# Kernel tuning notes

Measured on AMD Instinct MI355X. Metric: run time of the kernel, lower is better.

## Reference

```python
import jax, jax.numpy as jnp
import numpy as np

D, B, N, DIM, H, DH, MLP = 6, 4, 1024, 768, 12, 64, 3072
SCALE = DH ** -0.5
EPS = 1e-5


def setup_inputs() -> dict:
    key = jax.random.key(0)
    ks = jax.random.split(key, 5)
    s = 0.02
    return {
        "x": jax.random.normal(ks[0], (B, N, DIM), jnp.float32),
        "ln1_g": jnp.ones((D, DIM), jnp.float32),
        "ln1_b": jnp.zeros((D, DIM), jnp.float32),
        "wqkv": jax.random.normal(ks[1], (D, DIM, 3 * H * DH), jnp.float32) * s,
        "wo": jax.random.normal(ks[2], (D, H * DH, DIM), jnp.float32) * s,
        "bo": jnp.zeros((D, DIM), jnp.float32),
        "ln2_g": jnp.ones((D, DIM), jnp.float32),
        "ln2_b": jnp.zeros((D, DIM), jnp.float32),
        "w1": jax.random.normal(ks[3], (D, DIM, MLP), jnp.float32) * s,
        "b1": jnp.zeros((D, MLP), jnp.float32),
        "w2": jax.random.normal(ks[4], (D, MLP, DIM), jnp.float32) * s,
        "b2": jnp.zeros((D, DIM), jnp.float32),
    }


def _ln(h, g, b):
    m = h.mean(-1, keepdims=True)
    v = h.var(-1, keepdims=True)  # biased, matches torch LayerNorm
    return (h - m) / jnp.sqrt(v + EPS) * g + b


def _heads(t):
    # [b, n, h*d] -> [b, h, n, d]
    return t.reshape(B, N, H, DH).transpose(0, 2, 1, 3)


def reference(x, ln1_g, ln1_b, wqkv, wo, bo, ln2_g, ln2_b, w1, b1, w2, b2):
    def step(carry, p):
        xc, _, _ = carry
        g1, be1, Wqkv, Wo, Bo, g2, be2, W1, B1, W2, B2 = p
        h = _ln(xc, g1, be1)
        q, k, v = jnp.split(h @ Wqkv, 3, axis=-1)
        q, k, v = _heads(q), _heads(k), _heads(v)
        attn = jax.nn.softmax(jnp.einsum('bhid,bhjd->bhij', q, k) * SCALE, axis=-1)
        out = jnp.einsum('bhij,bhjd->bhid', attn, v)
        out = out.transpose(0, 2, 1, 3).reshape(B, N, H * DH)
        xc = xc + out @ Wo + Bo
        h2 = _ln(xc, g2, be2)
        xc = xc + jax.nn.gelu(h2 @ W1 + B1, approximate=False) @ W2 + B2
        return (xc, k, v), None

    kv0 = jnp.zeros((B, H, N, DH), x.dtype)
    (xf, k, v), _ = jax.lax.scan(
        step, (x, kv0, kv0),
        (ln1_g, ln1_b, wqkv, wo, bo, ln2_g, ln2_b, w1, b1, w2, b2))
    return xf, k, v
```

## Files before the change

kernel.cpp:

```cpp
#include <hip/hip_runtime.h>
#include <hip/hip_bf16.h>
#include <math.h>

typedef __bf16 bf16;
typedef __bf16 bf16x8 __attribute__((ext_vector_type(8)));
typedef float f32x4 __attribute__((ext_vector_type(4)));

enum { EPI_QKV = 0, EPI_GELU = 1 };

__device__ __forceinline__ void gload16(const void* g, void* s) {
  __builtin_amdgcn_global_load_lds((__attribute__((address_space(1))) void*)g,
                                   (__attribute__((address_space(3))) void*)s, 16, 0, 0);
}

#define MFMA16(a, b, c) __builtin_amdgcn_mfma_f32_16x16x32_bf16((a), (b), (c), 0, 0, 0)

__device__ __forceinline__ void xcd_swizzle(int& bx, int& by) {
  const int gx = gridDim.x, nwg = gx * gridDim.y;
  int bid = blockIdx.y * gx + blockIdx.x;
  if ((nwg & 7) == 0) bid = (bid & 7) * (nwg >> 3) + (bid >> 3);
  bx = bid % gx;
  by = bid / gx;
}

__global__ __launch_bounds__(256) void cast_x(const float* __restrict__ x,
                                              float* __restrict__ xq) {
  const int i = (blockIdx.x * 256 + threadIdx.x) * 4;
  float4 v = *(const float4*)(x + i);
  v.x = (float)(bf16)v.x; v.y = (float)(bf16)v.y;
  v.z = (float)(bf16)v.z; v.w = (float)(bf16)v.w;
  *(float4*)(xq + i) = v;
}

__global__ __launch_bounds__(256) void wconv_all(
    const float* __restrict__ wqkv, const float* __restrict__ wo,
    const float* __restrict__ w1, const float* __restrict__ w2,
    bf16* __restrict__ qkvT, bf16* __restrict__ woT,
    bf16* __restrict__ w1T, bf16* __restrict__ w2T, int lfix) {
  __shared__ float tile[64][65];
  const int bid = blockIdx.x, t = threadIdx.x;
  int l, r;
  if (lfix < 0) { l = bid / 1728; r = bid % 1728; } else { l = lfix; r = bid; }
  const int lo = (lfix < 0) ? l : 0;
  const float* W; bf16* Wt; int K, N, tt;
  if (r < 432)       { W = wqkv + (size_t)l * 768 * 2304; Wt = qkvT + (size_t)lo * 2304 * 768; K = 768;  N = 2304; tt = r; }
  else if (r < 576)  { W = wo   + (size_t)l * 768 * 768;  Wt = woT  + (size_t)lo * 768 * 768;  K = 768;  N = 768;  tt = r - 432; }
  else if (r < 1152) { W = w1   + (size_t)l * 768 * 3072; Wt = w1T  + (size_t)lo * 3072 * 768; K = 768;  N = 3072; tt = r - 576; }
  else               { W = w2   + (size_t)l * 3072 * 768; Wt = w2T  + (size_t)lo * 768 * 3072; K = 3072; N = 768;  tt = r - 1152; }
  const int ntx = N >> 6;
  const int n0 = (tt % ntx) * 64, k0 = (tt / ntx) * 64;
  const int cx = (t & 15) * 4, ry = t >> 4;
#pragma unroll
  for (int pp = 0; pp < 4; ++pp) {
    const int row = ry + pp * 16;
    const float4 v = *(const float4*)(W + (size_t)(k0 + row) * N + n0 + cx);
    tile[row][cx] = v.x; tile[row][cx + 1] = v.y;
    tile[row][cx + 2] = v.z; tile[row][cx + 3] = v.w;
  }
  __syncthreads();
#pragma unroll
  for (int it = 0; it < 2; ++it) {
    const int c = it * 256 + t;
    const int n = c >> 3, kc = (c & 7) * 8;
    bf16x8 v;
#pragma unroll
    for (int j = 0; j < 8; ++j) v[j] = (bf16)tile[kc + j][n];
    *(bf16x8*)(Wt + (size_t)(n0 + n) * K + k0 + kc) = v;
  }
}

__global__ __launch_bounds__(256) void ln_kernel(const float* __restrict__ x,
                                                 const float* __restrict__ g,
                                                 const float* __restrict__ b,
                                                 bf16* __restrict__ out) {
  const int row = blockIdx.x, t = threadIdx.x;
  const float* xr = x + (size_t)row * 768;
  float v0 = xr[t], v1 = xr[t + 256], v2 = xr[t + 512];
  float s = v0 + v1 + v2, sq = v0 * v0 + v1 * v1 + v2 * v2;
#pragma unroll
  for (int m = 32; m; m >>= 1) { s += __shfl_xor(s, m); sq += __shfl_xor(sq, m); }
  __shared__ float rs[4], rq[4];
  const int w = t >> 6;
  if ((t & 63) == 0) { rs[w] = s; rq[w] = sq; }
  __syncthreads();
  s = rs[0] + rs[1] + rs[2] + rs[3];
  sq = rq[0] + rq[1] + rq[2] + rq[3];
  const float mean = s * (1.f / 768.f);
  const float var = sq * (1.f / 768.f) - mean * mean;
  const float rstd = rsqrtf(var + 1e-5f);
  bf16* orow = out + (size_t)row * 768;
  orow[t]       = (bf16)((v0 - mean) * rstd * g[t]       + b[t]);
  orow[t + 256] = (bf16)((v1 - mean) * rstd * g[t + 256] + b[t + 256]);
  orow[t + 512] = (bf16)((v2 - mean) * rstd * g[t + 512] + b[t + 512]);
}

template <int EPI>
__global__ __launch_bounds__(256) void gemm_s(
    const bf16* __restrict__ A, const bf16* __restrict__ Bt,
    const float* __restrict__ bias, bf16* __restrict__ Cb,
    bf16* __restrict__ qo, bf16* __restrict__ ko_, bf16* __restrict__ vo,
    float* __restrict__ kf, float* __restrict__ vf, int wf,
    int M, int Nc, int K) {
  __shared__ __align__(16) char lds[2][2][8192];
  const int t = threadIdx.x, lane = t & 63, w = t >> 6;
  const int wr = w >> 1, wc = w & 1;
  int bx, by;
  xcd_swizzle(bx, by);
  const size_t m0 = (size_t)by * 128, n0 = (size_t)bx * 128;

  const char* ab[2]; const char* bb[2];
#pragma unroll
  for (int r = 0; r < 2; ++r) {
    int c = r * 256 + t;
    ab[r] = (const char*)(A + (m0 + (c >> 2)) * (size_t)K) + (c & 3) * 16;
    bb[r] = (const char*)(Bt + (n0 + (c >> 2)) * (size_t)K) + (c & 3) * 16;
  }

  f32x4 acc[4][4] = {};

  auto stage = [&](int buf, int tt) {
#pragma unroll
    for (int r = 0; r < 2; ++r) {
      gload16(ab[r] + (size_t)tt * 64, &lds[buf][0][r * 4096 + w * 1024]);
      gload16(bb[r] + (size_t)tt * 64, &lds[buf][1][r * 4096 + w * 1024]);
    }
  };
  auto compute = [&](int buf) {
    const char* As = lds[buf][0];
    const char* Bs = lds[buf][1];
    const int ko = (lane >> 4) * 16;
    bf16x8 af[4], fb[4];
#pragma unroll
    for (int i = 0; i < 4; ++i) {
      af[i] = *(const bf16x8*)(As + (wr * 64 + i * 16 + (lane & 15)) * 64 + ko);
      fb[i] = *(const bf16x8*)(Bs + (wc * 64 + i * 16 + (lane & 15)) * 64 + ko);
    }
#pragma unroll
    for (int mi = 0; mi < 4; ++mi)
#pragma unroll
      for (int ni = 0; ni < 4; ++ni)
        acc[mi][ni] = MFMA16(af[mi], fb[ni], acc[mi][ni]);
  };

  const int NT = K >> 5;
  stage(0, 0);
  __syncthreads();
  int cur = 0;
  for (int tt = 1; tt < NT; ++tt) {
    stage(cur ^ 1, tt);
    compute(cur);
    __syncthreads();
    cur ^= 1;
  }
  compute(cur);

#pragma unroll
  for (int mi = 0; mi < 4; ++mi) {
#pragma unroll
    for (int i = 0; i < 4; ++i) {
      size_t row = m0 + wr * 64 + mi * 16 + ((lane >> 4) << 2) + i;
#pragma unroll
      for (int ni = 0; ni < 4; ++ni) {
        size_t col = n0 + wc * 64 + ni * 16 + (lane & 15);
        float v = acc[mi][ni][i];
        if (EPI == EPI_GELU) {
          v += bias[col];
          v = 0.5f * v * (1.f + erff(v * 0.70710678118f));
          Cb[row * (size_t)Nc + col] = (bf16)v;
        } else {
          int b = (int)(row >> 10), n = (int)(row & 1023);
          int which = (int)col >= 1536 ? 2 : ((int)col >= 768 ? 1 : 0);
          int hd = (int)col - which * 768;
          int hh = hd >> 6, d = hd & 63;
          size_t dst = ((size_t)(b * 12 + hh) * 1024 + n) * 64 + d;
          if (which == 0) {
            qo[dst] = (bf16)(v * 0.125f);
          } else if (which == 1) {
            ko_[dst] = (bf16)v;
            if (wf) kf[dst] = v;
          } else {
            vo[dst] = (bf16)v;
            if (wf) vf[dst] = v;
          }
        }
      }
    }
  }
}

__global__ __launch_bounds__(256) void gemm64_s(
    const bf16* __restrict__ A, const bf16* __restrict__ Bt,
    const float* __restrict__ bias, const float* __restrict__ res,
    float* __restrict__ Cf, int M, int Nc, int K) {
  __shared__ __align__(16) char lds[2][12288];
  const int t = threadIdx.x, lane = t & 63, w = t >> 6;
  const int wr = w >> 1, wc = w & 1;
  const int l15 = lane & 15, l4 = lane >> 4;
  int bx, by;
  xcd_swizzle(bx, by);
  const size_t m0 = (size_t)by * 64, n0 = (size_t)bx * 128;

  const char* ab = (const char*)(A + (m0 + (t >> 2)) * (size_t)K) + (t & 3) * 16;
  const char* b0 = (const char*)(Bt + (n0 + (t >> 2)) * (size_t)K) + (t & 3) * 16;
  const char* b1 = (const char*)(Bt + (n0 + 64 + (t >> 2)) * (size_t)K) + (t & 3) * 16;

  f32x4 acc[2][4] = {};

  auto stage = [&](int buf, int tt) {
    gload16(ab + (size_t)tt * 64, &lds[buf][t * 16]);
    gload16(b0 + (size_t)tt * 64, &lds[buf][4096 + t * 16]);
    gload16(b1 + (size_t)tt * 64, &lds[buf][8192 + t * 16]);
  };
  auto compute = [&](int buf) {
    const char* L = lds[buf];
    const int ko = l4 * 16;
    bf16x8 fa[2], fb[4];
#pragma unroll
    for (int mi = 0; mi < 2; ++mi)
      fa[mi] = *(const bf16x8*)(L + (wr * 32 + mi * 16 + l15) * 64 + ko);
#pragma unroll
    for (int ni = 0; ni < 4; ++ni)
      fb[ni] = *(const bf16x8*)(L + 4096 + (wc * 64 + ni * 16 + l15) * 64 + ko);
#pragma unroll
    for (int mi = 0; mi < 2; ++mi)
#pragma unroll
      for (int ni = 0; ni < 4; ++ni)
        acc[mi][ni] = MFMA16(fa[mi], fb[ni], acc[mi][ni]);
  };

  const int NT = K >> 5;
  stage(0, 0);
  __syncthreads();
  int cur = 0;
  for (int tt = 1; tt < NT; ++tt) {
    stage(cur ^ 1, tt);
    compute(cur);
    __syncthreads();
    cur ^= 1;
  }
  compute(cur);

#pragma unroll
  for (int mi = 0; mi < 2; ++mi) {
#pragma unroll
    for (int i = 0; i < 4; ++i) {
      size_t row = m0 + wr * 32 + mi * 16 + l4 * 4 + i;
#pragma unroll
      for (int ni = 0; ni < 4; ++ni) {
        size_t col = n0 + wc * 64 + ni * 16 + l15;
        float v = acc[mi][ni][i] + bias[col] + res[row * (size_t)Nc + col];
        Cf[row * (size_t)Nc + col] = v;
      }
    }
  }
}

__global__ __launch_bounds__(256) void vtrans(const bf16* __restrict__ v,
                                              bf16* __restrict__ vT) {
  __shared__ bf16 tile[32][33];
  const int tx = threadIdx.x, ty = threadIdx.y;
  const int bh = blockIdx.x, n0 = blockIdx.y * 32, d0 = blockIdx.z * 32;
  const bf16* vb = v + (size_t)bh * 1024 * 64;
  bf16* vTb = vT + (size_t)bh * 64 * 1024;
#pragma unroll
  for (int r = 0; r < 4; ++r)
    tile[ty + r * 8][tx] = vb[(size_t)(n0 + ty + r * 8) * 64 + d0 + tx];
  __syncthreads();
#pragma unroll
  for (int r = 0; r < 4; ++r)
    vTb[(size_t)(d0 + ty + r * 8) * 1024 + n0 + tx] = tile[tx][ty + r * 8];
}

__global__ __launch_bounds__(64) void attn_kernel(const bf16* __restrict__ q,
                                                  const bf16* __restrict__ k,
                                                  const bf16* __restrict__ vT,
                                                  bf16* __restrict__ out) {
  __shared__ __align__(16) char Ks[16384];
  __shared__ __align__(16) char Vs[16384];
  char* Ps = Ks;
  const int bh = blockIdx.x, qb = blockIdx.y;
  const int lane = threadIdx.x & 63;
  const int l15 = lane & 15, l4 = lane >> 4;

  const char* kp = (const char*)(k + (size_t)bh * 1024 * 64);
  const char* vp = (const char*)(vT + (size_t)bh * 64 * 1024);

  const char* kb0 = kp + (lane >> 3) * 128 + (((lane & 7) ^ ((lane >> 3) & 7)) * 16);
  const int vr0 = lane >> 4;
  const char* vb0 = vp + (size_t)vr0 * 2048 + (((lane & 15) ^ vr0) * 16);
  const char* vb1 = vp + (size_t)(vr0 + 4) * 2048 + (((lane & 15) ^ (vr0 + 4)) * 16);

  bf16x8 aq[2][2];
  {
    const bf16* qbase = q + ((size_t)bh * 1024 + qb * 32) * 64;
#pragma unroll
    for (int mi = 0; mi < 2; ++mi)
#pragma unroll
      for (int ks = 0; ks < 2; ++ks)
        aq[mi][ks] = *(const bf16x8*)(qbase + (mi * 16 + l15) * 64 + ks * 32 + l4 * 8);
  }

  bf16x8 vones;
#pragma unroll
  for (int j = 0; j < 8; ++j) vones[j] = (bf16)1.0f;

  f32x4 oacc[2][4] = {};
  f32x4 lacc[2] = {};
  float mrun[2][4];
#pragma unroll
  for (int mi = 0; mi < 2; ++mi)
#pragma unroll
    for (int i = 0; i < 4; ++i) mrun[mi][i] = -1e30f;

  for (int kb = 0; kb < 8; ++kb) {
    const char* ksrc = kb0 + (size_t)kb * 16384;
#pragma unroll
    for (int r = 0; r < 16; ++r)
      gload16(ksrc + r * 1024, &Ks[r * 1024]);
    const char* vsrc0 = vb0 + kb * 256;
    const char* vsrc1 = vb1 + kb * 256;
#pragma unroll
    for (int r = 0; r < 8; ++r) {
      gload16(vsrc0 + (size_t)r * 16384, &Vs[r * 2048]);
      gload16(vsrc1 + (size_t)r * 16384, &Vs[r * 2048 + 1024]);
    }
    asm volatile("s_waitcnt vmcnt(16)" ::: "memory");
    __builtin_amdgcn_sched_barrier(0);

    f32x4 sacc[2][8] = {};
#pragma unroll
    for (int ks = 0; ks < 2; ++ks) {
#pragma unroll
      for (int ni = 0; ni < 8; ++ni) {
        const int rr = ni * 16 + l15;
        const bf16x8 bk = *(const bf16x8*)(Ks + rr * 128 + (((ks * 4 + l4) ^ (rr & 7)) * 16));
        sacc[0][ni] = MFMA16(aq[0][ks], bk, sacc[0][ni]);
        sacc[1][ni] = MFMA16(aq[1][ks], bk, sacc[1][ni]);
      }
    }

#pragma unroll
    for (int mi = 0; mi < 2; ++mi) {
#pragma unroll
      for (int i = 0; i < 4; ++i) {
        float mx = sacc[mi][0][i];
#pragma unroll
        for (int ni = 1; ni < 8; ++ni) mx = fmaxf(mx, sacc[mi][ni][i]);
#pragma unroll
        for (int sh = 8; sh; sh >>= 1) mx = fmaxf(mx, __shfl_xor(mx, sh));
        float mnew = fmaxf(mrun[mi][i], mx);
        float alpha = __expf(mrun[mi][i] - mnew);
        mrun[mi][i] = mnew;
#pragma unroll
        for (int ni = 0; ni < 8; ++ni)
          sacc[mi][ni][i] = __expf(sacc[mi][ni][i] - mnew);
#pragma unroll
        for (int ni = 0; ni < 4; ++ni) oacc[mi][ni][i] *= alpha;
        lacc[mi][i] *= alpha;
      }
    }

#pragma unroll
    for (int mi = 0; mi < 2; ++mi)
#pragma unroll
      for (int i = 0; i < 4; ++i) {
        int rowl = mi * 16 + l4 * 4 + i;
        char* prp = Ps + rowl * 256;
        int sw = rowl & 7;
#pragma unroll
        for (int ni = 0; ni < 8; ++ni) {
          int col = ni * 16 + l15;
          *(bf16*)(prp + (((col >> 3) ^ sw) * 16) + (col & 7) * 2) = (bf16)sacc[mi][ni][i];
        }
      }

    asm volatile("s_waitcnt vmcnt(0)" ::: "memory");
    __builtin_amdgcn_sched_barrier(0);

    const int prow0 = l15, prow1 = 16 + l15;
#pragma unroll
    for (int ks = 0; ks < 4; ++ks) {
      const bf16x8 ap0 = *(const bf16x8*)(Ps + prow0 * 256 + (((ks * 4 + l4) ^ (prow0 & 7)) * 16));
      const bf16x8 ap1 = *(const bf16x8*)(Ps + prow1 * 256 + (((ks * 4 + l4) ^ (prow1 & 7)) * 16));
#pragma unroll
      for (int ni = 0; ni < 4; ++ni) {
        const int vr = ni * 16 + l15;
        const bf16x8 bv = *(const bf16x8*)(Vs + vr * 256 + (((ks * 4 + l4) ^ (vr & 7)) * 16));
        oacc[0][ni] = MFMA16(ap0, bv, oacc[0][ni]);
        oacc[1][ni] = MFMA16(ap1, bv, oacc[1][ni]);
      }
      lacc[0] = MFMA16(ap0, vones, lacc[0]);
      lacc[1] = MFMA16(ap1, vones, lacc[1]);
    }
  }

  const int b = bh / 12, hh = bh % 12;
#pragma unroll
  for (int mi = 0; mi < 2; ++mi)
#pragma unroll
    for (int i = 0; i < 4; ++i) {
      int n = qb * 32 + mi * 16 + l4 * 4 + i;
      float inv = 1.f / lacc[mi][i];
      bf16* orow = out + ((size_t)b * 1024 + n) * 768 + hh * 64;
#pragma unroll
      for (int ni = 0; ni < 4; ++ni)
        orow[ni * 16 + l15] = (bf16)(oacc[mi][ni][i] * inv);
    }
}

extern "C" void kernel_launch(void* const* d_in, const int* in_sizes, int n_in,
                              void* d_out, int out_size, void* d_ws, size_t ws_size,
                              hipStream_t stream) {
  (void)in_sizes; (void)n_in; (void)out_size;
  const float* x_in = (const float*)d_in[0];
  const float* ln1g = (const float*)d_in[1];
  const float* ln1b = (const float*)d_in[2];
  const float* wqkv = (const float*)d_in[3];
  const float* wo   = (const float*)d_in[4];
  const float* bo   = (const float*)d_in[5];
  const float* ln2g = (const float*)d_in[6];
  const float* ln2b = (const float*)d_in[7];
  const float* w1   = (const float*)d_in[8];
  const float* b1   = (const float*)d_in[9];
  const float* w2   = (const float*)d_in[10];
  const float* b2   = (const float*)d_in[11];

  float* outx = (float*)d_out;
  float* outk = outx + (size_t)4096 * 768;
  float* outv = outk + (size_t)4096 * 768;

  char* p = (char*)d_ws;
  auto take = [&](size_t bytes) {
    char* r = p;
    p += (bytes + 255) & ~(size_t)255;
    return r;
  };
  float* xw   = (float*)take((size_t)4096 * 768 * 4);
  bf16*  h    = (bf16*)take((size_t)4096 * 768 * 2);
  bf16*  mbuf = (bf16*)take((size_t)4096 * 3072 * 2);
  bf16*  qbuf = (bf16*)take((size_t)4096 * 768 * 2);
  bf16*  kbuf = (bf16*)take((size_t)4096 * 768 * 2);
  bf16*  vbuf = (bf16*)take((size_t)4096 * 768 * 2);
  bf16*  vTb  = (bf16*)take((size_t)4096 * 768 * 2);
  bf16*  abuf = (bf16*)take((size_t)4096 * 768 * 2);

  const size_t wq1 = (size_t)2304 * 768, wo1 = (size_t)768 * 768,
               w11 = (size_t)3072 * 768, w21 = (size_t)768 * 3072;
  const size_t used = (size_t)(p - (char*)d_ws);
  const size_t wbytes = (wq1 + wo1 + w11 + w21) * 2;
  const bool hoist = ws_size >= used + 6 * wbytes + 8192;
  const int nl = hoist ? 6 : 1;
  bf16* qkvT = (bf16*)take(wq1 * 2 * nl);
  bf16* woT  = (bf16*)take(wo1 * 2 * nl);
  bf16* w1T  = (bf16*)take(w11 * 2 * nl);
  bf16* w2T  = (bf16*)take(w21 * 2 * nl);

  cast_x<<<3072, 256, 0, stream>>>(x_in, xw);
  if (hoist)
    wconv_all<<<10368, 256, 0, stream>>>(wqkv, wo, w1, w2, qkvT, woT, w1T, w2T, -1);

  for (int l = 0; l < 6; ++l) {
    if (!hoist)
      wconv_all<<<1728, 256, 0, stream>>>(wqkv, wo, w1, w2, qkvT, woT, w1T, w2T, l);
    bf16* qkL = qkvT + (hoist ? (size_t)l * wq1 : 0);
    bf16* woL = woT  + (hoist ? (size_t)l * wo1 : 0);
    bf16* w1L = w1T  + (hoist ? (size_t)l * w11 : 0);
    bf16* w2L = w2T  + (hoist ? (size_t)l * w21 : 0);

    ln_kernel<<<4096, 256, 0, stream>>>(xw, ln1g + l * 768, ln1b + l * 768, h);
    gemm_s<EPI_QKV><<<dim3(18, 32), 256, 0, stream>>>(
        h, qkL, nullptr, nullptr, qbuf, kbuf, vbuf, outk, outv, l == 5 ? 1 : 0,
        4096, 2304, 768);
    vtrans<<<dim3(48, 32, 2), dim3(32, 8), 0, stream>>>(vbuf, vTb);
    attn_kernel<<<dim3(48, 32), 64, 0, stream>>>(qbuf, kbuf, vTb, abuf);
    gemm64_s<<<dim3(6, 64), 256, 0, stream>>>(
        abuf, woL, bo + l * 768, xw, xw, 4096, 768, 768);
    ln_kernel<<<4096, 256, 0, stream>>>(xw, ln2g + l * 768, ln2b + l * 768, h);
    gemm_s<EPI_GELU><<<dim3(24, 32), 256, 0, stream>>>(
        h, w1L, b1 + l * 3072, mbuf, nullptr, nullptr, nullptr, nullptr, nullptr, 0,
        4096, 3072, 768);
    gemm64_s<<<dim3(6, 64), 256, 0, stream>>>(
        mbuf, w2L, b2 + l * 768, xw, (l == 5) ? outx : xw, 4096, 768, 3072);
  }
}
```

Measured before the change: 1.270 ms.

## Split attention over key halves with a separate log-sum-exp combine kernel

```diff
diff --git a/kernel.cpp b/kernel.cpp
--- a/kernel.cpp
+++ b/kernel.cpp
@@ -271,24 +271,28 @@
     vTb[(size_t)(d0 + ty + r * 8) * 1024 + n0 + tx] = tile[tx][ty + r * 8];
 }
 
-__global__ __launch_bounds__(64) void attn_kernel(const bf16* __restrict__ q,
-                                                  const bf16* __restrict__ k,
-                                                  const bf16* __restrict__ vT,
-                                                  bf16* __restrict__ out) {
+__global__ __launch_bounds__(64) void attn_main(const bf16* __restrict__ q,
+                                                const bf16* __restrict__ k,
+                                                const bf16* __restrict__ vT,
+                                                float* __restrict__ pO,
+                                                float* __restrict__ pM,
+                                                float* __restrict__ pL) {
   __shared__ __align__(16) char Ks[16384];
   __shared__ __align__(16) char Vs[16384];
   char* Ps = Ks;
-  const int bh = blockIdx.x, qb = blockIdx.y;
+  const int bh = blockIdx.x, qb = blockIdx.y, half = blockIdx.z;
   const int lane = threadIdx.x & 63;
   const int l15 = lane & 15, l4 = lane >> 4;
 
   const char* kp = (const char*)(k + (size_t)bh * 1024 * 64);
   const char* vp = (const char*)(vT + (size_t)bh * 64 * 1024);
 
-  const char* kb0 = kp + (lane >> 3) * 128 + (((lane & 7) ^ ((lane >> 3) & 7)) * 16);
+  const char* kb0 = kp + (lane >> 3) * 128 + (((lane & 7) ^ ((lane >> 3) & 7)) * 16)
+                  + (size_t)half * 4 * 16384;
   const int vr0 = lane >> 4;
-  const char* vb0 = vp + (size_t)vr0 * 2048 + (((lane & 15) ^ vr0) * 16);
-  const char* vb1 = vp + (size_t)(vr0 + 4) * 2048 + (((lane & 15) ^ (vr0 + 4)) * 16);
+  const char* vb0 = vp + (size_t)vr0 * 2048 + (((lane & 15) ^ vr0) * 16) + half * 4 * 256;
+  const char* vb1 = vp + (size_t)(vr0 + 4) * 2048 + (((lane & 15) ^ (vr0 + 4)) * 16)
+                  + half * 4 * 256;
 
   bf16x8 aq[2][2];
   {
@@ -312,13 +316,14 @@
 #pragma unroll
     for (int i = 0; i < 4; ++i) mrun[mi][i] = -1e30f;
 
-  for (int kb = 0; kb < 8; ++kb) {
-    const char* ksrc = kb0 + (size_t)kb * 16384;
+#pragma unroll
+  for (int jb = 0; jb < 4; ++jb) {
+    const char* ksrc = kb0 + (size_t)jb * 16384;
 #pragma unroll
     for (int r = 0; r < 16; ++r)
       gload16(ksrc + r * 1024, &Ks[r * 1024]);
-    const char* vsrc0 = vb0 + kb * 256;
-    const char* vsrc1 = vb1 + kb * 256;
+    const char* vsrc0 = vb0 + jb * 256;
+    const char* vsrc1 = vb1 + jb * 256;
 #pragma unroll
     for (int r = 0; r < 8; ++r) {
       gload16(vsrc0 + (size_t)r * 16384, &Vs[r * 2048]);
@@ -394,18 +399,47 @@
     }
   }
 
+  const size_t pb = ((size_t)half * 1536 + bh * 32 + qb) * 32;
+#pragma unroll
+  for (int mi = 0; mi < 2; ++mi)
+#pragma unroll
+    for (int i = 0; i < 4; ++i) {
+      const int row = mi * 16 + l4 * 4 + i;
+      float* po = pO + (pb + row) * 64;
+#pragma unroll
+      for (int ni = 0; ni < 4; ++ni)
+        po[ni * 16 + l15] = oacc[mi][ni][i];
+      if (l15 == 0) {
+        pM[pb + row] = mrun[mi][i];
+        pL[pb + row] = lacc[mi][i];
+      }
+    }
+}
+
+__global__ __launch_bounds__(256) void attn_combine(const float* __restrict__ pO,
+                                                    const float* __restrict__ pM,
+                                                    const float* __restrict__ pL,
+                                                    bf16* __restrict__ out) {
+  const int blk = blockIdx.x;
+  const int bh = blk >> 5, qb = blk & 31;
+  const int t = threadIdx.x;
+  const int row = t >> 3, d0 = (t & 7) * 8;
+  const size_t base = (size_t)blk * 32 + row;
+  const float m0 = pM[base], m1 = pM[49152 + base];
+  const float M = fmaxf(m0, m1);
+  const float s0 = __expf(m0 - M), s1 = __expf(m1 - M);
+  const float L = pL[base] * s0 + pL[49152 + base] * s1;
+  const float inv = 1.f / L;
+  const float* p0 = pO + base * 64 + d0;
+  const float* p1 = pO + (size_t)49152 * 64 + base * 64 + d0;
   const int b = bh / 12, hh = bh % 12;
-#pragma unroll
-  for (int mi = 0; mi < 2; ++mi)
-#pragma unroll
-    for (int i = 0; i < 4; ++i) {
-      int n = qb * 32 + mi * 16 + l4 * 4 + i;
-      float inv = 1.f / lacc[mi][i];
-      bf16* orow = out + ((size_t)b * 1024 + n) * 768 + hh * 64;
-#pragma unroll
-      for (int ni = 0; ni < 4; ++ni)
-        orow[ni * 16 + l15] = (bf16)(oacc[mi][ni][i] * inv);
-    }
+  const int n = qb * 32 + row;
+  bf16* orow = out + ((size_t)b * 1024 + n) * 768 + hh * 64 + d0;
+  bf16x8 ov;
+#pragma unroll
+  for (int j = 0; j < 8; ++j)
+    ov[j] = (bf16)((p0[j] * s0 + p1[j] * s1) * inv);
+  *(bf16x8*)orow = ov;
 }
 
 extern "C" void kernel_launch(void* const* d_in, const int* in_sizes, int n_in,
@@ -443,6 +477,9 @@
   bf16*  vbuf = (bf16*)take((size_t)4096 * 768 * 2);
   bf16*  vTb  = (bf16*)take((size_t)4096 * 768 * 2);
   bf16*  abuf = (bf16*)take((size_t)4096 * 768 * 2);
+  float* pM   = (float*)take((size_t)2 * 49152 * 4);
+  float* pL   = (float*)take((size_t)2 * 49152 * 4);
+  float* pO   = (float*)mbuf;
 
   const size_t wq1 = (size_t)2304 * 768, wo1 = (size_t)768 * 768,
                w11 = (size_t)3072 * 768, w21 = (size_t)768 * 3072;
@@ -472,7 +509,8 @@
         h, qkL, nullptr, nullptr, qbuf, kbuf, vbuf, outk, outv, l == 5 ? 1 : 0,
         4096, 2304, 768);
     vtrans<<<dim3(48, 32, 2), dim3(32, 8), 0, stream>>>(vbuf, vTb);
-    attn_kernel<<<dim3(48, 32), 64, 0, stream>>>(qbuf, kbuf, vTb, abuf);
+    attn_main<<<dim3(48, 32, 2), 64, 0, stream>>>(qbuf, kbuf, vTb, pO, pM, pL);
+    attn_combine<<<1536, 256, 0, stream>>>(pO, pM, pL, abuf);
     gemm64_s<<<dim3(6, 64), 256, 0, stream>>>(
         abuf, woL, bo + l * 768, xw, xw, 4096, 768, 768);
     ln_kernel<<<4096, 256, 0, stream>>>(xw, ln2g + l * 768, ln2b + l * 768, h);
```

Result: faster. 1.235 ms (median of 2 runs) (-2.8%).
